# Performance work log

Measured on AMD Instinct MI355X. Metric: run time of the kernel, lower is better.

The kernel has to match this reference:

```python
import jax, jax.numpy as jnp
import numpy as np

T, E, H = 65536, 512, 512  # seq_len, embedding_size, hidden_size (kernel_size=2)


def setup_inputs() -> dict:
    key = jax.random.key(0)
    k1, k2 = jax.random.split(key)
    x = jax.random.normal(k1, (T, E), dtype=jnp.float32)
    # nn.Linear(2*E, 3*H): weight [3H, 2E], bias [3H]. Store transposed for x @ W.
    W = jax.random.normal(k2, (2 * E, 3 * H), dtype=jnp.float32) * 0.02
    b = jnp.zeros((3 * H,), dtype=jnp.float32)
    return {"input": x, "W": W, "b": b}


def reference(input, W, b):
    x = input
    t, e = x.shape
    h_dim = W.shape[1] // 3
    # Shift input by one step (zero-padded) and concat: conv over kernel_size=2 window.
    x_prev = jnp.concatenate([jnp.zeros((1, e), x.dtype), x[:-1]], axis=0)  # [T, E]
    gates = jnp.concatenate([x, x_prev], axis=1) @ W + b  # [T, 3H]
    z = jnp.tanh(gates[:, :h_dim])                # cell candidate
    f = jax.nn.sigmoid(gates[:, h_dim:2 * h_dim])  # forget gate
    o = jax.nn.sigmoid(gates[:, 2 * h_dim:])       # output gate

    # fo-pool recurrence: c_t = f_t * c_{t-1} + (1 - f_t) * z_t ; h_t = o_t * c_t
    def step(c, zfo):
        z_t, f_t, o_t = zfo
        c_new = f_t * c + (1.0 - f_t) * z_t
        return c_new, (c_new, o_t * c_new)

    c0 = jnp.zeros((h_dim,), x.dtype)
    _, (cells, hiddens) = jax.lax.scan(step, c0, (z, f, o))
    # Match torch: (hidden_temp [T,H], h [1,H], c [1,H])
    return hiddens, hiddens[-1:], cells[-1:]
```

## Files before the change

kernel.cpp:

```cpp
#include <hip/hip_runtime.h>


#define T_LEN 65536
#define H3    1536
#define LC    64
#define NCHUNK 1024

typedef float f32x4 __attribute__((ext_vector_type(4)));
typedef short bf16x8 __attribute__((ext_vector_type(8)));

__device__ __forceinline__ unsigned short f2bf(float f) {
    unsigned int x = __builtin_bit_cast(unsigned int, f);
    x += 0x7fffu + ((x >> 16) & 1u);
    return (unsigned short)(x >> 16);
}
__device__ __forceinline__ float bf2f(unsigned short u) {
    return __builtin_bit_cast(float, ((unsigned int)u) << 16);
}
__device__ __forceinline__ float fsig(float x) {
    return __builtin_amdgcn_rcpf(1.f + __builtin_amdgcn_exp2f(-1.44269504f * x));
}
__device__ __forceinline__ float ftanh(float x) {
    return 2.f * __builtin_amdgcn_rcpf(1.f + __builtin_amdgcn_exp2f(-2.88539008f * x)) - 1.f;
}

__device__ __forceinline__ void gload_lds16(const void* g, void* l) {
    __builtin_amdgcn_global_load_lds((const __attribute__((address_space(1))) void*)g,
                                     (__attribute__((address_space(3))) void*)l, 16, 0, 0);
}

__global__ void prep_x(const float* __restrict__ x, unsigned short* __restrict__ xp) {
    const long long nq = (512LL + (long long)T_LEN * 512) / 4;
    for (long long q = (long long)blockIdx.x * blockDim.x + threadIdx.x; q < nq;
         q += (long long)gridDim.x * blockDim.x) {
        ushort4 u;
        if (q < 128) {
            u.x = 0; u.y = 0; u.z = 0; u.w = 0;
        } else {
            const float4 v = *reinterpret_cast<const float4*>(x + q * 4 - 512);
            u.x = f2bf(v.x); u.y = f2bf(v.y); u.z = f2bf(v.z); u.w = f2bf(v.w);
        }
        *reinterpret_cast<ushort4*>(xp + q * 4) = u;
    }
}

__global__ void prep_w(const float* __restrict__ W, unsigned short* __restrict__ Wt) {
    const int n_el = 1024 * H3;
    for (int i = blockIdx.x * blockDim.x + threadIdx.x; i < n_el;
         i += gridDim.x * blockDim.x) {
        const int k = i / H3, n = i - k * H3;
        Wt[n * 1024 + k] = f2bf(W[i]);
    }
}

__global__ __launch_bounds__(256, 2) void gemm_gates(
    const unsigned short* __restrict__ xp,
    const unsigned short* __restrict__ Wt,
    const float* __restrict__ bias,
    unsigned short* __restrict__ zfo)
{
    __shared__ unsigned short Alds[3][128 * 32];
    __shared__ unsigned short Blds[3][256 * 32];

    const int tid  = threadIdx.x;
    const int lane = tid & 63;
    const int w    = tid >> 6;
    const int wm   = w >> 1, wn = w & 1;

    const int flat = blockIdx.y * gridDim.x + blockIdx.x;
    const int idx  = (flat & 7) * 384 + (flat >> 3);
    const int nb   = (idx % 6) * 256;
    const long long t0 = (long long)(idx / 6) * 128;

    const int srow_l = lane >> 2;
    const int scol   = (((lane & 3) ^ ((lane >> 3) & 3)) * 8);

    const unsigned short* gA = xp + (t0 + w * 16 + srow_l) * 512 + 512 + scol;
    const unsigned short* gB = Wt + (long long)(nb + w * 16 + srow_l) * 1024 + scol;

    auto stage = [&](unsigned short* Al, unsigned short* Bl) {
        gload_lds16(gA,              Al + (w * 16) * 32);
        gload_lds16(gA + 64 * 512,   Al + (64 + w * 16) * 32);
        gload_lds16(gB,              Bl + (w * 16) * 32);
        gload_lds16(gB + 64 * 1024,  Bl + (64 + w * 16) * 32);
        gload_lds16(gB + 128 * 1024, Bl + (128 + w * 16) * 32);
        gload_lds16(gB + 192 * 1024, Bl + (192 + w * 16) * 32);
    };

    const int arow  = lane & 15;
    const int swzco = (((lane >> 4) ^ ((arow >> 1) & 3)) * 8);

    f32x4 acc[4][8] = {};

    auto compute = [&](const unsigned short* Al, const unsigned short* Bl) {
        bf16x8 af[4], bfr[8];
        #pragma unroll
        for (int m = 0; m < 4; ++m)
            af[m] = *reinterpret_cast<const bf16x8*>(Al + (wm * 64 + m * 16 + arow) * 32 + swzco);
        #pragma unroll
        for (int n = 0; n < 8; ++n)
            bfr[n] = *reinterpret_cast<const bf16x8*>(Bl + (wn * 128 + n * 16 + arow) * 32 + swzco);
        #pragma unroll
        for (int n = 0; n < 8; ++n)
            #pragma unroll
            for (int m = 0; m < 4; ++m)
                acc[m][n] = __builtin_amdgcn_mfma_f32_16x16x32_bf16(af[m], bfr[n], acc[m][n], 0, 0, 0);
    };

    stage(Alds[0], Blds[0]); gA += 32; gB += 32;
    stage(Alds[1], Blds[1]); gA += 32; gB += 32;
    asm volatile("s_waitcnt vmcnt(6)" ::: "memory");
    __builtin_amdgcn_s_barrier();

    for (int kt = 0; kt < 30; kt += 3) {
        {
            stage(Alds[2], Blds[2]);
            gA += (kt + 2 == 15) ? -992 : 32;  gB += 32;
            compute(Alds[0], Blds[0]);
            asm volatile("s_waitcnt vmcnt(6)" ::: "memory");
            __builtin_amdgcn_s_barrier();
        }
        {
            stage(Alds[0], Blds[0]);
            gA += (kt + 3 == 15) ? -992 : 32;  gB += 32;
            compute(Alds[1], Blds[1]);
            asm volatile("s_waitcnt vmcnt(6)" ::: "memory");
            __builtin_amdgcn_s_barrier();
        }
        {
            stage(Alds[1], Blds[1]);
            gA += (kt + 4 == 15) ? -992 : 32;  gB += 32;
            compute(Alds[2], Blds[2]);
            asm volatile("s_waitcnt vmcnt(6)" ::: "memory");
            __builtin_amdgcn_s_barrier();
        }
    }
    compute(Alds[0], Blds[0]);
    asm volatile("s_waitcnt vmcnt(0)" ::: "memory");
    __builtin_amdgcn_s_barrier();
    compute(Alds[1], Blds[1]);

    const int cls = nb >> 9;
    #pragma unroll
    for (int n = 0; n < 8; ++n) {
        const int col = nb + wn * 128 + n * 16 + arow;
        const float bn_ = bias[col];
        #pragma unroll
        for (int m = 0; m < 4; ++m) {
            const long long row0 = t0 + wm * 64 + m * 16 + (lane >> 4) * 4;
            #pragma unroll
            for (int j = 0; j < 4; ++j) {
                float v = acc[m][n][j] + bn_;
                v = (cls == 0) ? ftanh(v) : fsig(v);
                zfo[(row0 + j) * H3 + col] = f2bf(v);
            }
        }
    }
}

__global__ void scan_pass1(const unsigned short* __restrict__ zfo,
                           float* __restrict__ P, float* __restrict__ L) {
    const int chunk = blockIdx.x;
    const int c4    = threadIdx.x;
    const unsigned short* base = zfo + (long long)chunk * LC * H3 + c4 * 4;
    float c[4] = {0.f, 0.f, 0.f, 0.f};
    float p[4] = {1.f, 1.f, 1.f, 1.f};
    for (int t = 0; t < LC; ++t) {
        const unsigned short* row = base + t * H3;
        const ushort4 uz = *reinterpret_cast<const ushort4*>(row);
        const ushort4 uf = *reinterpret_cast<const ushort4*>(row + 512);
        const float z[4] = {bf2f(uz.x), bf2f(uz.y), bf2f(uz.z), bf2f(uz.w)};
        const float f[4] = {bf2f(uf.x), bf2f(uf.y), bf2f(uf.z), bf2f(uf.w)};
        #pragma unroll
        for (int j = 0; j < 4; ++j) {
            c[j] = fmaf(f[j], c[j] - z[j], z[j]);
            p[j] *= f[j];
        }
    }
    #pragma unroll
    for (int j = 0; j < 4; ++j) {
        P[chunk * 512 + c4 * 4 + j] = p[j];
        L[chunk * 512 + c4 * 4 + j] = c[j];
    }
}

__global__ __launch_bounds__(1024) void scan_pass2(
    const float* __restrict__ P, const float* __restrict__ L,
    float* __restrict__ carry, float* __restrict__ out) {
    const int ch = blockIdx.x;
    const int k  = threadIdx.x;
    __shared__ float sP[1024], sL[1024];
    float p = P[k * 512 + ch];
    float l = L[k * 512 + ch];
    sP[k] = p; sL[k] = l;
    __syncthreads();
    for (int d = 1; d < 1024; d <<= 1) {
        float pp = 1.f, ll = 0.f;
        if (k >= d) { pp = sP[k - d]; ll = sL[k - d]; }
        __syncthreads();
        l = fmaf(p, ll, l);
        p = p * pp;
        sP[k] = p; sL[k] = l;
        __syncthreads();
    }
    carry[k * 512 + ch] = (k == 0) ? 0.f : sL[k - 1];
    if (k == 1023) out[(long long)T_LEN * 512 + 512 + ch] = l;
}

__global__ void scan_pass3(const unsigned short* __restrict__ zfo,
                           const float* __restrict__ carry,
                           float* __restrict__ out) {
    const int chunk = blockIdx.x;
    const int c4    = threadIdx.x;
    const unsigned short* base = zfo + (long long)chunk * LC * H3 + c4 * 4;
    float c[4], h[4] = {0.f, 0.f, 0.f, 0.f};
    #pragma unroll
    for (int j = 0; j < 4; ++j) c[j] = carry[chunk * 512 + c4 * 4 + j];
    float4* outp = reinterpret_cast<float4*>(out + (long long)chunk * LC * 512) + c4;
    for (int t = 0; t < LC; ++t) {
        const unsigned short* row = base + t * H3;
        const ushort4 uz = *reinterpret_cast<const ushort4*>(row);
        const ushort4 uf = *reinterpret_cast<const ushort4*>(row + 512);
        const ushort4 uo = *reinterpret_cast<const ushort4*>(row + 1024);
        const float z[4] = {bf2f(uz.x), bf2f(uz.y), bf2f(uz.z), bf2f(uz.w)};
        const float f[4] = {bf2f(uf.x), bf2f(uf.y), bf2f(uf.z), bf2f(uf.w)};
        const float o[4] = {bf2f(uo.x), bf2f(uo.y), bf2f(uo.z), bf2f(uo.w)};
        #pragma unroll
        for (int j = 0; j < 4; ++j) {
            c[j] = fmaf(f[j], c[j] - z[j], z[j]);
            h[j] = o[j] * c[j];
        }
        float4 hv; hv.x = h[0]; hv.y = h[1]; hv.z = h[2]; hv.w = h[3];
        outp[t * 128] = hv;
    }
    if (chunk == NCHUNK - 1) {
        #pragma unroll
        for (int j = 0; j < 4; ++j)
            out[(long long)T_LEN * 512 + c4 * 4 + j] = h[j];
    }
}

extern "C" void kernel_launch(void* const* d_in, const int* in_sizes, int n_in,
                              void* d_out, int out_size, void* d_ws, size_t ws_size,
                              hipStream_t stream) {
    const float* x = (const float*)d_in[0];
    const float* W = (const float*)d_in[1];
    const float* b = (const float*)d_in[2];
    float* out = (float*)d_out;

    char* ws = (char*)d_ws;
    unsigned short* xp  = (unsigned short*)(ws);
    unsigned short* Wt  = (unsigned short*)(ws + 67110912LL);
    unsigned short* zfo = (unsigned short*)(ws + 70256640LL);
    float* P     = (float*)(ws);
    float* L     = (float*)(ws + 4194304LL);
    float* carry = (float*)(ws + 8388608LL);

    prep_x<<<4096, 256, 0, stream>>>(x, xp);
    prep_w<<<768, 256, 0, stream>>>(W, Wt);

    dim3 gg(H3 / 256, T_LEN / 128, 1);
    gemm_gates<<<gg, 256, 0, stream>>>(xp, Wt, b, zfo);

    scan_pass1<<<NCHUNK, 128, 0, stream>>>(zfo, P, L);
    scan_pass2<<<512, 1024, 0, stream>>>(P, L, carry, out);
    scan_pass3<<<NCHUNK, 128, 0, stream>>>(zfo, carry, out);
}
```

Before: 382.9 us.

## Split GEMM staging into 4-deep A prefetch and double-buffered B

The gates GEMM's triple-buffered joint A/B pipeline is replaced by separate ones: activation tiles are prefetched three K-steps ahead in four LDS buffers, and weight tiles are double-buffered one step ahead. The aim is to hide latency on the streamed activations, which are not reused across blocks, while cutting total LDS per block. The cost is a shallower prefetch for the weight tiles, which must now arrive within a single compute step. That could stall if they are not cache resident.

```diff
diff --git a/kernel.cpp b/kernel.cpp
--- a/kernel.cpp
+++ b/kernel.cpp
@@ -28,6 +28,10 @@
     __builtin_amdgcn_global_load_lds((const __attribute__((address_space(1))) void*)g,
                                      (__attribute__((address_space(3))) void*)l, 16, 0, 0);
 }
+
+#define VM2()   asm volatile("s_waitcnt vmcnt(2)" ::: "memory")
+#define VM0()   asm volatile("s_waitcnt vmcnt(0)" ::: "memory")
+#define BARX()  __builtin_amdgcn_s_barrier()
 
 __global__ void prep_x(const float* __restrict__ x, unsigned short* __restrict__ xp) {
     const long long nq = (512LL + (long long)T_LEN * 512) / 4;
@@ -59,8 +63,8 @@
     const float* __restrict__ bias,
     unsigned short* __restrict__ zfo)
 {
-    __shared__ unsigned short Alds[3][128 * 32];
-    __shared__ unsigned short Blds[3][256 * 32];
+    __shared__ unsigned short Alds[4][128 * 32];
+    __shared__ unsigned short Blds[2][256 * 32];
 
     const int tid  = threadIdx.x;
     const int lane = tid & 63;
@@ -78,9 +82,11 @@
     const unsigned short* gA = xp + (t0 + w * 16 + srow_l) * 512 + 512 + scol;
     const unsigned short* gB = Wt + (long long)(nb + w * 16 + srow_l) * 1024 + scol;
 
-    auto stage = [&](unsigned short* Al, unsigned short* Bl) {
+    auto stageA = [&](unsigned short* Al) {
         gload_lds16(gA,              Al + (w * 16) * 32);
         gload_lds16(gA + 64 * 512,   Al + (64 + w * 16) * 32);
+    };
+    auto stageB = [&](unsigned short* Bl) {
         gload_lds16(gB,              Bl + (w * 16) * 32);
         gload_lds16(gB + 64 * 1024,  Bl + (64 + w * 16) * 32);
         gload_lds16(gB + 128 * 1024, Bl + (128 + w * 16) * 32);
@@ -107,38 +113,41 @@
                 acc[m][n] = __builtin_amdgcn_mfma_f32_16x16x32_bf16(af[m], bfr[n], acc[m][n], 0, 0, 0);
     };
 
-    stage(Alds[0], Blds[0]); gA += 32; gB += 32;
-    stage(Alds[1], Blds[1]); gA += 32; gB += 32;
-    asm volatile("s_waitcnt vmcnt(6)" ::: "memory");
-    __builtin_amdgcn_s_barrier();
-
-    for (int kt = 0; kt < 30; kt += 3) {
-        {
-            stage(Alds[2], Blds[2]);
-            gA += (kt + 2 == 15) ? -992 : 32;  gB += 32;
-            compute(Alds[0], Blds[0]);
-            asm volatile("s_waitcnt vmcnt(6)" ::: "memory");
-            __builtin_amdgcn_s_barrier();
-        }
-        {
-            stage(Alds[0], Blds[0]);
-            gA += (kt + 3 == 15) ? -992 : 32;  gB += 32;
-            compute(Alds[1], Blds[1]);
-            asm volatile("s_waitcnt vmcnt(6)" ::: "memory");
-            __builtin_amdgcn_s_barrier();
-        }
-        {
-            stage(Alds[1], Blds[1]);
-            gA += (kt + 4 == 15) ? -992 : 32;  gB += 32;
-            compute(Alds[2], Blds[2]);
-            asm volatile("s_waitcnt vmcnt(6)" ::: "memory");
-            __builtin_amdgcn_s_barrier();
-        }
-    }
-    compute(Alds[0], Blds[0]);
-    asm volatile("s_waitcnt vmcnt(0)" ::: "memory");
-    __builtin_amdgcn_s_barrier();
-    compute(Alds[1], Blds[1]);
+    stageB(Blds[0]); gB += 32;
+    stageA(Alds[0]); gA += 32;
+    stageA(Alds[1]); gA += 32;
+    stageA(Alds[2]); gA += 32;
+    asm volatile("s_waitcnt vmcnt(4)" ::: "memory");
+    BARX();
+
+    for (int base = 0; base < 28; base += 4) {
+        #pragma unroll
+        for (int k = 0; k < 4; ++k) {
+            stageB(Blds[(k + 1) & 1]); gB += 32;
+            stageA(Alds[(k + 3) & 3]);
+            gA += (base + k == 12) ? -992 : 32;
+            compute(Alds[k & 3], Blds[k & 1]);
+            VM2();
+            BARX();
+        }
+    }
+    {
+        stageB(Blds[1]); gB += 32;
+        stageA(Alds[3]);
+        compute(Alds[0], Blds[0]);
+        VM2(); BARX();
+    }
+    {
+        stageB(Blds[0]); gB += 32;
+        compute(Alds[1], Blds[1]);
+        VM0(); BARX();
+    }
+    {
+        stageB(Blds[1]);
+        compute(Alds[2], Blds[0]);
+        VM0(); BARX();
+    }
+    compute(Alds[3], Blds[1]);
 
     const int cls = nb >> 9;
     #pragma unroll
```

Measured after the change: 377.8 us. About the same (-1.3%).

## Fuse three-pass chunked scan into single-pass decoupled look-back scan

Applied to the files above, without the earlier changes.

Replaces the three scan kernels (per-chunk aggregate, cross-chunk prefix, and re-scan) with one kernel that uses decoupled look-back. Each block publishes its aggregate and inclusive prefix through status flags, then resolves its carry by walking back over predecessor blocks. This removes two kernel launches and the global round trip for the P/L/carry arrays. In exchange it adds spin-waiting on atomics and a memset of the flags, and it depends on earlier blocks making forward progress.

```diff
diff --git a/kernel.cpp b/kernel.cpp
--- a/kernel.cpp
+++ b/kernel.cpp
@@ -28,6 +28,10 @@
     __builtin_amdgcn_global_load_lds((const __attribute__((address_space(1))) void*)g,
                                      (__attribute__((address_space(3))) void*)l, 16, 0, 0);
 }
+
+#define VM6()   asm volatile("s_waitcnt vmcnt(6)" ::: "memory")
+#define VM0()   asm volatile("s_waitcnt vmcnt(0)" ::: "memory")
+#define BARX()  __builtin_amdgcn_s_barrier()
 
 __global__ void prep_x(const float* __restrict__ x, unsigned short* __restrict__ xp) {
     const long long nq = (512LL + (long long)T_LEN * 512) / 4;
@@ -109,35 +113,35 @@
 
     stage(Alds[0], Blds[0]); gA += 32; gB += 32;
     stage(Alds[1], Blds[1]); gA += 32; gB += 32;
-    asm volatile("s_waitcnt vmcnt(6)" ::: "memory");
-    __builtin_amdgcn_s_barrier();
+    VM6();
+    BARX();
 
     for (int kt = 0; kt < 30; kt += 3) {
         {
             stage(Alds[2], Blds[2]);
             gA += (kt + 2 == 15) ? -992 : 32;  gB += 32;
             compute(Alds[0], Blds[0]);
-            asm volatile("s_waitcnt vmcnt(6)" ::: "memory");
-            __builtin_amdgcn_s_barrier();
+            VM6();
+            BARX();
         }
         {
             stage(Alds[0], Blds[0]);
             gA += (kt + 3 == 15) ? -992 : 32;  gB += 32;
             compute(Alds[1], Blds[1]);
-            asm volatile("s_waitcnt vmcnt(6)" ::: "memory");
-            __builtin_amdgcn_s_barrier();
+            VM6();
+            BARX();
         }
         {
             stage(Alds[1], Blds[1]);
             gA += (kt + 4 == 15) ? -992 : 32;  gB += 32;
             compute(Alds[2], Blds[2]);
-            asm volatile("s_waitcnt vmcnt(6)" ::: "memory");
-            __builtin_amdgcn_s_barrier();
+            VM6();
+            BARX();
         }
     }
     compute(Alds[0], Blds[0]);
-    asm volatile("s_waitcnt vmcnt(0)" ::: "memory");
-    __builtin_amdgcn_s_barrier();
+    VM0();
+    BARX();
     compute(Alds[1], Blds[1]);
 
     const int cls = nb >> 9;
@@ -158,11 +162,17 @@
     }
 }
 
-__global__ void scan_pass1(const unsigned short* __restrict__ zfo,
-                           float* __restrict__ P, float* __restrict__ L) {
-    const int chunk = blockIdx.x;
-    const int c4    = threadIdx.x;
-    const unsigned short* base = zfo + (long long)chunk * LC * H3 + c4 * 4;
+__global__ __launch_bounds__(128) void scan_fused(
+    const unsigned short* __restrict__ zfo,
+    float* __restrict__ aggP, float* __restrict__ aggL,
+    float* __restrict__ pref, int* __restrict__ status,
+    float* __restrict__ out)
+{
+    const int b   = blockIdx.x;
+    const int c4  = threadIdx.x;
+    const int chb = c4 * 4;
+    const unsigned short* base = zfo + (long long)b * LC * H3 + chb;
+
     float c[4] = {0.f, 0.f, 0.f, 0.f};
     float p[4] = {1.f, 1.f, 1.f, 1.f};
     for (int t = 0; t < LC; ++t) {
@@ -177,46 +187,73 @@
             p[j] *= f[j];
         }
     }
-    #pragma unroll
-    for (int j = 0; j < 4; ++j) {
-        P[chunk * 512 + c4 * 4 + j] = p[j];
-        L[chunk * 512 + c4 * 4 + j] = c[j];
-    }
-}
-
-__global__ __launch_bounds__(1024) void scan_pass2(
-    const float* __restrict__ P, const float* __restrict__ L,
-    float* __restrict__ carry, float* __restrict__ out) {
-    const int ch = blockIdx.x;
-    const int k  = threadIdx.x;
-    __shared__ float sP[1024], sL[1024];
-    float p = P[k * 512 + ch];
-    float l = L[k * 512 + ch];
-    sP[k] = p; sL[k] = l;
-    __syncthreads();
-    for (int d = 1; d < 1024; d <<= 1) {
-        float pp = 1.f, ll = 0.f;
-        if (k >= d) { pp = sP[k - d]; ll = sL[k - d]; }
+
+    float C[4];
+    if (b == 0) {
+        #pragma unroll
+        for (int j = 0; j < 4; ++j) pref[chb + j] = c[j];
+        __threadfence();
         __syncthreads();
-        l = fmaf(p, ll, l);
-        p = p * pp;
-        sP[k] = p; sL[k] = l;
+        if (c4 == 0)
+            __hip_atomic_store(&status[0], 2, __ATOMIC_RELEASE, __HIP_MEMORY_SCOPE_AGENT);
+        C[0] = C[1] = C[2] = C[3] = 0.f;
+    } else {
+        #pragma unroll
+        for (int j = 0; j < 4; ++j) {
+            aggP[b * 512 + chb + j] = p[j];
+            aggL[b * 512 + chb + j] = c[j];
+        }
+        __threadfence();
         __syncthreads();
-    }
-    carry[k * 512 + ch] = (k == 0) ? 0.f : sL[k - 1];
-    if (k == 1023) out[(long long)T_LEN * 512 + 512 + ch] = l;
-}
-
-__global__ void scan_pass3(const unsigned short* __restrict__ zfo,
-                           const float* __restrict__ carry,
-                           float* __restrict__ out) {
-    const int chunk = blockIdx.x;
-    const int c4    = threadIdx.x;
-    const unsigned short* base = zfo + (long long)chunk * LC * H3 + c4 * 4;
-    float c[4], h[4] = {0.f, 0.f, 0.f, 0.f};
-    #pragma unroll
-    for (int j = 0; j < 4; ++j) c[j] = carry[chunk * 512 + c4 * 4 + j];
-    float4* outp = reinterpret_cast<float4*>(out + (long long)chunk * LC * 512) + c4;
+        if (c4 == 0)
+            __hip_atomic_store(&status[b], 1, __ATOMIC_RELEASE, __HIP_MEMORY_SCOPE_AGENT);
+
+        __shared__ int st;
+        float Pa[4] = {1.f, 1.f, 1.f, 1.f};
+        float La[4] = {0.f, 0.f, 0.f, 0.f};
+        int j = b - 1;
+        for (;;) {
+            if (c4 == 0) {
+                int s;
+                do {
+                    s = __hip_atomic_load(&status[j], __ATOMIC_ACQUIRE, __HIP_MEMORY_SCOPE_AGENT);
+                } while (s == 0);
+                st = s;
+            }
+            __syncthreads();
+            const int s = st;
+            if (s == 2) {
+                #pragma unroll
+                for (int k = 0; k < 4; ++k)
+                    C[k] = fmaf(Pa[k], pref[j * 512 + chb + k], La[k]);
+                break;
+            }
+            #pragma unroll
+            for (int k = 0; k < 4; ++k) {
+                const float Pj = aggP[j * 512 + chb + k];
+                const float Lj = aggL[j * 512 + chb + k];
+                La[k] = fmaf(Pa[k], Lj, La[k]);
+                Pa[k] *= Pj;
+            }
+            --j;
+            if (j < 0) {
+                #pragma unroll
+                for (int k = 0; k < 4; ++k) C[k] = La[k];
+                break;
+            }
+            __syncthreads();
+        }
+        #pragma unroll
+        for (int k = 0; k < 4; ++k) pref[b * 512 + chb + k] = fmaf(p[k], C[k], c[k]);
+        __threadfence();
+        __syncthreads();
+        if (c4 == 0)
+            __hip_atomic_store(&status[b], 2, __ATOMIC_RELEASE, __HIP_MEMORY_SCOPE_AGENT);
+    }
+
+    float cc[4] = {C[0], C[1], C[2], C[3]};
+    float h[4]  = {0.f, 0.f, 0.f, 0.f};
+    float4* outp = reinterpret_cast<float4*>(out + (long long)b * LC * 512) + c4;
     for (int t = 0; t < LC; ++t) {
         const unsigned short* row = base + t * H3;
         const ushort4 uz = *reinterpret_cast<const ushort4*>(row);
@@ -227,16 +264,18 @@
         const float o[4] = {bf2f(uo.x), bf2f(uo.y), bf2f(uo.z), bf2f(uo.w)};
         #pragma unroll
         for (int j = 0; j < 4; ++j) {
-            c[j] = fmaf(f[j], c[j] - z[j], z[j]);
-            h[j] = o[j] * c[j];
+            cc[j] = fmaf(f[j], cc[j] - z[j], z[j]);
+            h[j]  = o[j] * cc[j];
         }
         float4 hv; hv.x = h[0]; hv.y = h[1]; hv.z = h[2]; hv.w = h[3];
         outp[t * 128] = hv;
     }
-    if (chunk == NCHUNK - 1) {
-        #pragma unroll
-        for (int j = 0; j < 4; ++j)
-            out[(long long)T_LEN * 512 + c4 * 4 + j] = h[j];
+    if (b == NCHUNK - 1) {
+        #pragma unroll
+        for (int j = 0; j < 4; ++j) {
+            out[(long long)T_LEN * 512 + chb + j]       = h[j];
+            out[(long long)T_LEN * 512 + 512 + chb + j] = cc[j];
+        }
     }
 }
 
@@ -252,9 +291,10 @@
     unsigned short* xp  = (unsigned short*)(ws);
     unsigned short* Wt  = (unsigned short*)(ws + 67110912LL);
     unsigned short* zfo = (unsigned short*)(ws + 70256640LL);
-    float* P     = (float*)(ws);
-    float* L     = (float*)(ws + 4194304LL);
-    float* carry = (float*)(ws + 8388608LL);
+    int*   status = (int*)(ws);
+    float* aggP   = (float*)(ws + 1048576LL);
+    float* aggL   = (float*)(ws + 3145728LL);
+    float* pref   = (float*)(ws + 5242880LL);
 
     prep_x<<<4096, 256, 0, stream>>>(x, xp);
     prep_w<<<768, 256, 0, stream>>>(W, Wt);
@@ -262,7 +302,7 @@
     dim3 gg(H3 / 256, T_LEN / 128, 1);
     gemm_gates<<<gg, 256, 0, stream>>>(xp, Wt, b, zfo);
 
-    scan_pass1<<<NCHUNK, 128, 0, stream>>>(zfo, P, L);
-    scan_pass2<<<512, 1024, 0, stream>>>(P, L, carry, out);
-    scan_pass3<<<NCHUNK, 128, 0, stream>>>(zfo, carry, out);
-}
+    hipMemsetAsync(status, 0, NCHUNK * sizeof(int), stream);
+
+    scan_fused<<<NCHUNK, 128, 0, stream>>>(zfo, aggP, aggL, pref, status, out);
+}
```

Result: slower. 877.5 us (+129.2%).
